# Kernel tuning notes

Measured on AMD Instinct MI355X. Metric: run time of the kernel, lower is better.

The kernel has to match this reference:

```python
import jax, jax.numpy as jnp
import numpy as np

B, C, H, Wd = 4, 144, 64, 64
CM = 64          # mid channels (planes[1..3])
K, PAD = 5, 2    # proj_kernel_size unfold
EPS = 1e-5       # BatchNorm eps


def _bn(x, g, b, m, v, axis=1):
    sh = [1] * x.ndim
    sh[axis] = -1
    return (x - m.reshape(sh)) * (g.reshape(sh) * jax.lax.rsqrt(v.reshape(sh) + EPS)) + b.reshape(sh)


def setup_inputs():
    key = jax.random.key(0)
    ks = jax.random.split(key, 24)
    def w(k, shape, s=0.1):
        return jax.random.normal(k, shape, dtype=jnp.float32) * s
    inp = {
        'x': jax.random.normal(ks[0], (B, C, H, Wd), dtype=jnp.float32),
        'w_in': w(ks[1], (CM, C)),
        'g_in': 1.0 + w(ks[2], (CM,)), 'b_in': w(ks[3], (CM,)),
        'm_in': w(ks[4], (CM,)), 'v_in': jax.random.uniform(ks[5], (CM,), minval=0.5, maxval=1.5),
        'w1': w(ks[6], (CM, CM, 3, 3)),
        'g1': 1.0 + w(ks[7], (CM,)), 'b1': w(ks[8], (CM,)),
        'm1': w(ks[9], (CM,)), 'v1': jax.random.uniform(ks[10], (CM,), minval=0.5, maxval=1.5),
        'w2': w(ks[11], (CM, CM, 3, 3)),
        'g2': 1.0 + w(ks[12], (CM,)), 'b2': w(ks[13], (CM,)),
        'm2': w(ks[14], (CM,)), 'v2': jax.random.uniform(ks[15], (CM,), minval=0.5, maxval=1.5),
        'w_out': w(ks[16], (C, CM)),
        'g_out': 1.0 + w(ks[17], (C,)), 'b_out': w(ks[18], (C,)),
        'm_out': w(ks[19], (C,)), 'v_out': jax.random.uniform(ks[20], (C,), minval=0.5, maxval=1.5),
    }
    return inp


def _forward(x, w_in, g_in, b_in, m_in, v_in, w1, g1, b1, m1, v1,
             w2, g2, b2, m2, v2, w_out, g_out, b_out, m_out, v_out):
    b, c, h, wd = x.shape
    # F.normalize over channel dim (L2, eps=1e-12)
    x = x / jnp.maximum(jnp.sqrt(jnp.sum(x * x, axis=1, keepdims=True)), 1e-12)
    # 5x5 unfold (im2col), pad 2 -> patches [b, c, K*K, h, w] (row-major (kh,kw) like torch)
    xp = jnp.pad(x, ((0, 0), (0, 0), (PAD, PAD), (PAD, PAD)))
    patches = jnp.stack([xp[:, :, i:i + h, j:j + wd]
                         for i in range(K) for j in range(K)], axis=2)
    # elementwise correlation with center pixel, reorder -> [b, c, h*w, K*K]
    y = patches * x[:, :, None, :, :]
    y = jnp.moveaxis(y, 2, -1).reshape(b, c, h * wd, K * K)
    # conv1x1_in + BN + ReLU (1x1 conv == channel matmul)
    z = jnp.einsum('oc,bcpk->bopk', w_in, y)
    z = jax.nn.relu(_bn(z, g_in, b_in, m_in, v_in, axis=1))
    cm = z.shape[1]
    # Conv3d kernel (1,3,3) VALID == 2D 3x3 conv per spatial position: fold h*w into batch
    z = z.reshape(b, cm, h * wd, K, K).transpose(0, 2, 1, 3, 4).reshape(b * h * wd, cm, K, K)
    dn = ('NCHW', 'OIHW', 'NCHW')
    z = jax.lax.conv_general_dilated(z, w1, (1, 1), 'VALID', dimension_numbers=dn)
    z = jax.nn.relu(_bn(z, g1, b1, m1, v1, axis=1))  # [b*hw, cm, 3, 3]
    z = jax.lax.conv_general_dilated(z, w2, (1, 1), 'VALID', dimension_numbers=dn)
    z = jax.nn.relu(_bn(z, g2, b2, m2, v2, axis=1))  # [b*hw, cm, 1, 1]
    z = z.reshape(b, h * wd, cm).transpose(0, 2, 1).reshape(b, cm, h, wd)
    # conv1x1_out + BN (final layer: no ReLU)
    out = jnp.einsum('oc,bchw->bohw', w_out, z)
    return _bn(out, g_out, b_out, m_out, v_out, axis=1)


def reference(x, w_in, g_in, b_in, m_in, v_in, w1, g1, b1, m1, v1,
              w2, g2, b2, m2, v2, w_out, g_out, b_out, m_out, v_out):
    return _forward(x, w_in, g_in, b_in, m_in, v_in, w1, g1, b1, m1, v1,
                    w2, g2, b2, m2, v2, w_out, g_out, b_out, m_out, v_out)
```

## Files before the change

### kernel.cpp

```cpp
#include <hip/hip_runtime.h>

#define BB   4
#define CC   144
#define HW   4096
#define PTOT 16384
#define EPSB 1e-5f

typedef __bf16 bf16;
typedef __bf16 bf16x8 __attribute__((ext_vector_type(8)));
typedef float  f32x4  __attribute__((ext_vector_type(4)));
typedef unsigned short U16;
typedef U16 u16x4 __attribute__((ext_vector_type(4)));
typedef U16 u16x8 __attribute__((ext_vector_type(8)));

#define MFMA __builtin_amdgcn_mfma_f32_16x16x32_bf16

#define XN_OFF    0UL
#define WINF_OFF  76021760UL
#define W1F_OFF   76042240UL
#define W2F_OFF   76115968UL
#define WOUTF_OFF 76189696UL
#define BNP_OFF   76208128UL

__global__ __launch_bounds__(576) void k_prep(const float* __restrict__ x,
    const float* __restrict__ w_in, const float* __restrict__ w1,
    const float* __restrict__ w2,   const float* __restrict__ w_out,
    const float* g_in, const float* b_in, const float* m_in, const float* v_in,
    const float* g1,   const float* b1,   const float* m1,   const float* v1,
    const float* g2,   const float* b2,   const float* m2,   const float* v2,
    const float* g_out,const float* b_out,const float* m_out,const float* v_out,
    bf16* xn2, bf16* w_inf, bf16* w1f, bf16* w2f, bf16* w_outf, float* bnp)
{
    __shared__ float red[9][64];
    if (blockIdx.x < 256) {
        int bh = blockIdx.x;
        int t = threadIdx.x, w = t & 63, cq = t >> 6;
        const float* px = x + ((size_t)(bh >> 6) * CC) * HW + (bh & 63) * 64 + w;
        float vals[16];
        float s = 0.f;
        #pragma unroll
        for (int i = 0; i < 16; i++) {
            float v = px[(size_t)(cq * 16 + i) * HW];
            vals[i] = v; s += v * v;
        }
        red[cq][w] = s;
        __syncthreads();
        float tot = 0.f;
        #pragma unroll
        for (int q = 0; q < 9; q++) tot += red[q][w];
        float inv = 1.f / fmaxf(sqrtf(tot), 1e-12f);
        size_t p = (size_t)bh * 64 + w;
        #pragma unroll
        for (int k = 0; k < 2; k++) {
            int g = cq * 2 + k;
            u16x8 pk;
            #pragma unroll
            for (int j = 0; j < 8; j++) {
                bf16 v = (bf16)(vals[k * 8 + j] * inv);
                pk[j] = *(U16*)&v;
            }
            *(u16x8*)(xn2 + (((size_t)g) << 17) + p * 8) = pk;
        }
        return;
    }
    int t = (blockIdx.x - 256) * 576 + threadIdx.x;
    if (t < 10240) {
        int e = t, j = e & 7, lane = (e >> 3) & 63, r = e >> 9;
        int ks = r % 5, mt = r / 5;
        int o = mt * 16 + (lane & 15);
        int c = ks * 32 + ((lane >> 4) << 3) + j;
        float s = g_in[o] * rsqrtf(v_in[o] + EPSB);
        w_inf[e] = (c < 144) ? (bf16)(w_in[o * 144 + c] * s) : (bf16)0.f;
    } else if (t < 47104) {
        int e = t - 10240, j = e & 7, lane = (e >> 3) & 63, r = e >> 9;
        int ks = r % 18, mt = r / 18;
        int o = mt * 16 + (lane & 15);
        int k = ks * 32 + ((lane >> 4) << 3) + j;
        int ij = k >> 6, c = k & 63;
        float s = g1[o] * rsqrtf(v1[o] + EPSB);
        w1f[e] = (bf16)(w1[(o * 64 + c) * 9 + ij] * s);
    } else if (t < 83968) {
        int e = t - 47104, j = e & 7, lane = (e >> 3) & 63, r = e >> 9;
        int ks = r % 18, mt = r / 18;
        int o = mt * 16 + (lane & 15);
        int k = ks * 32 + ((lane >> 4) << 3) + j;
        int rs = k >> 6, c2 = k & 63;
        float s = g2[o] * rsqrtf(v2[o] + EPSB);
        w2f[e] = (bf16)(w2[o * 576 + c2 * 9 + rs] * s);
    } else if (t < 93184) {
        int e = t - 83968, j = e & 7, lane = (e >> 3) & 63, r = e >> 9;
        int ks = r & 1, mt = r >> 1;
        int o = mt * 16 + (lane & 15);
        int c = ks * 32 + ((lane >> 4) << 3) + j;
        float s = g_out[o] * rsqrtf(v_out[o] + EPSB);
        w_outf[e] = (bf16)(w_out[o * 64 + c] * s);
    } else if (t < 93856) {
        int i = t - 93184;
        const float *g, *bb, *mm, *vv; int c; bool is_t;
        if (i < 128)      { g=g_in; bb=b_in; mm=m_in; vv=v_in; c=i&63;        is_t=i>=64;  }
        else if (i < 256) { g=g1;   bb=b1;   mm=m1;   vv=v1;   c=(i-128)&63;  is_t=i>=192; }
        else if (i < 384) { g=g2;   bb=b2;   mm=m2;   vv=v2;   c=(i-256)&63;  is_t=i>=320; }
        else              { int ii=i-384; g=g_out; bb=b_out; mm=m_out; vv=v_out;
                            c = ii % 144; is_t = ii >= 144; }
        float s = g[c] * rsqrtf(vv[c] + EPSB);
        bnp[i] = is_t ? (bb[c] - mm[c] * s) : s;
    }
}

__global__ __launch_bounds__(256) void k_fused(const bf16* __restrict__ xn2,
        const bf16* __restrict__ w_inf, const bf16* __restrict__ w1f,
        const bf16* __restrict__ w2f,   const bf16* __restrict__ w_outf,
        const float* __restrict__ bnp,  float* __restrict__ out)
{
    __shared__ __align__(16) U16 lds[25600];
    U16* a2_lds = lds;
    U16* v3     = lds + 9216;

    const int LUT5c[9] = {0, 1, 2, 5, 6, 7, 10, 11, 12};

    int t = threadIdx.x, wid = t >> 6, lane = t & 63;
    int quad = lane >> 4, pl = lane & 15;
    int raw = blockIdx.x;
    int bid = (raw & 7) * 128 + (raw >> 3);
    int p0 = bid * 16;
    int b = p0 >> 12, h = (p0 >> 6) & 63, hw0 = p0 & 4095;
    int wc = (p0 & 63) + pl;

    bf16x8 af[4][5];
    #pragma unroll
    for (int mt = 0; mt < 4; mt++)
        #pragma unroll
        for (int ks = 0; ks < 5; ks++)
            af[mt][ks] = *(const bf16x8*)(w_inf + ((mt * 5 + ks) * 64 + lane) * 8);
    bf16x8 cfr[5];
    #pragma unroll
    for (int ks = 0; ks < 5; ks++) {
        int g = ks * 4 + quad;
        bf16x8 z = {};
        cfr[ks] = (g < 18) ? *(const bf16x8*)(xn2 + ((size_t)g << 17) + (size_t)(p0 + pl) * 8) : z;
    }
    f32x4 tv[4];
    #pragma unroll
    for (int mt = 0; mt < 4; mt++)
        tv[mt] = *(const f32x4*)&bnp[64 + mt * 16 + quad * 4];

    for (int kp = wid; kp < 25; kp += 4) {
        int kpr = kp / 5, kpc = kp - kpr * 5;
        int dh = kpr - 2, dw = kpc - 2;
        bool ok = ((unsigned)(h + dh) < 64u) && ((unsigned)(wc + dw) < 64u);
        size_t pn = (size_t)(p0 + dh * 64 + dw + pl);
        bf16x8 nv[5];
        #pragma unroll
        for (int ks = 0; ks < 5; ks++) {
            int g = ks * 4 + quad;
            bf16x8 z = {};
            nv[ks] = (ok && g < 18) ? *(const bf16x8*)(xn2 + ((size_t)g << 17) + pn * 8) : z;
        }
        f32x4 acc[4] = {};
        #pragma unroll
        for (int ks = 0; ks < 5; ks++) {
            bf16x8 bfr;
            #pragma unroll
            for (int j = 0; j < 8; j++)
                bfr[j] = (bf16)((float)nv[ks][j] * (float)cfr[ks][j]);
            #pragma unroll
            for (int mt = 0; mt < 4; mt++)
                acc[mt] = MFMA(af[mt][ks], bfr, acc[mt], 0, 0, 0);
        }
        int swb = kp * 3 + pl;
        #pragma unroll
        for (int mt = 0; mt < 4; mt++) {
            u16x4 pk;
            #pragma unroll
            for (int r = 0; r < 4; r++) {
                bf16 v = (bf16)fmaxf(acc[mt][r] + tv[mt][r], 0.f);
                pk[r] = *(U16*)&v;
            }
            int g0 = mt * 2 + (quad >> 1);
            int dst = pl * 1600 + kp * 64 + (((g0 + swb) & 7) << 3) + (quad & 1) * 4;
            *(u16x4*)&lds[dst] = pk;
        }
    }
    __syncthreads();

    u16x4 pk2[9];
    {
        int mt = wid;
        bf16x8 aaC[18];
        #pragma unroll
        for (int ks = 0; ks < 18; ks++)
            aaC[ks] = *(const bf16x8*)(w1f + ((mt * 18 + ks) * 64 + lane) * 8);
        f32x4 t1v = *(const f32x4*)&bnp[192 + mt * 16 + quad * 4];
        #pragma unroll
        for (int ch = 0; ch < 3; ch++) {
            f32x4 acc[3] = {};
            #pragma unroll
            for (int ks = 0; ks < 18; ks++) {
                int gb = (ks & 1) * 4 + quad;
                int l5 = LUT5c[ks >> 1];
                #pragma unroll
                for (int i = 0; i < 3; i++) {
                    int kpidx = l5 + LUT5c[ch * 3 + i];
                    int off = pl * 1600 + kpidx * 64 + (((gb + kpidx * 3 + pl) & 7) << 3);
                    bf16x8 bfr = *(const bf16x8*)&lds[off];
                    acc[i] = MFMA(aaC[ks], bfr, acc[i], 0, 0, 0);
                }
            }
            #pragma unroll
            for (int i = 0; i < 3; i++) {
                #pragma unroll
                for (int r = 0; r < 4; r++) {
                    bf16 v = (bf16)fmaxf(acc[i][r] + t1v[r], 0.f);
                    pk2[ch * 3 + i][r] = *(U16*)&v;
                }
            }
        }
    }
    __syncthreads();

    bf16x8 aaD[18];
    #pragma unroll
    for (int ks = 0; ks < 18; ks++)
        aaD[ks] = *(const bf16x8*)(w2f + ((wid * 18 + ks) * 64 + lane) * 8);
    {
        int mt = wid;
        #pragma unroll
        for (int rs = 0; rs < 9; rs++) {
            int c = rs * 8 + mt * 2 + (quad >> 1);
            int dst = pl * 576 + ((c >> 3) << 6) + ((((c & 7) + pl) & 7) << 3) + (quad & 1) * 4;
            *(u16x4*)&a2_lds[dst] = pk2[rs];
        }
    }
    __syncthreads();

    {
        int mt = wid;
        f32x4 acc3 = {};
        #pragma unroll
        for (int ks = 0; ks < 18; ks++) {
            int cg = ks * 4 + quad;
            int off = pl * 576 + ((cg >> 3) << 6) + ((((cg & 7) + pl) & 7) << 3);
            bf16x8 bfr = *(const bf16x8*)&a2_lds[off];
            acc3 = MFMA(aaD[ks], bfr, acc3, 0, 0, 0);
        }
        #pragma unroll
        for (int r = 0; r < 4; r++) {
            int o = mt * 16 + quad * 4 + r;
            bf16 yb = (bf16)fmaxf(acc3[r] + bnp[320 + o], 0.f);
            v3[pl * 64 + ((((o >> 3) + pl) & 7) << 3) + (o & 7)] = *(U16*)&yb;
        }
    }
    bf16x8 afrE[3][2];
    #pragma unroll
    for (int q = 0; q < 3; q++) {
        int mt = wid + q * 4;
        if (mt < 9) {
            afrE[q][0] = *(const bf16x8*)(w_outf + ((mt * 2 + 0) * 64 + lane) * 8);
            afrE[q][1] = *(const bf16x8*)(w_outf + ((mt * 2 + 1) * 64 + lane) * 8);
        }
    }
    __syncthreads();

    bf16x8 bfr0 = *(const bf16x8*)&v3[pl * 64 + (((quad + pl) & 7) << 3)];
    bf16x8 bfr1 = *(const bf16x8*)&v3[pl * 64 + ((((4 + quad) + pl) & 7) << 3)];
    #pragma unroll
    for (int q = 0; q < 3; q++) {
        int mt = wid + q * 4;
        if (mt < 9) {
            f32x4 accB = {};
            accB = MFMA(afrE[q][0], bfr0, accB, 0, 0, 0);
            accB = MFMA(afrE[q][1], bfr1, accB, 0, 0, 0);
            #pragma unroll
            for (int r = 0; r < 4; r++) {
                int oc = mt * 16 + quad * 4 + r;
                out[((size_t)(b * 144 + oc)) * 4096 + hw0 + pl] = accB[r] + bnp[528 + oc];
            }
        }
    }
}

extern "C" void kernel_launch(void* const* d_in, const int* in_sizes, int n_in,
                              void* d_out, int out_size, void* d_ws, size_t ws_size,
                              hipStream_t stream)
{
    const float* x     = (const float*)d_in[0];
    const float* w_in  = (const float*)d_in[1];
    const float* g_in  = (const float*)d_in[2];
    const float* b_in  = (const float*)d_in[3];
    const float* m_in  = (const float*)d_in[4];
    const float* v_in  = (const float*)d_in[5];
    const float* w1    = (const float*)d_in[6];
    const float* g1    = (const float*)d_in[7];
    const float* b1    = (const float*)d_in[8];
    const float* m1    = (const float*)d_in[9];
    const float* v1    = (const float*)d_in[10];
    const float* w2    = (const float*)d_in[11];
    const float* g2    = (const float*)d_in[12];
    const float* b2    = (const float*)d_in[13];
    const float* m2    = (const float*)d_in[14];
    const float* v2    = (const float*)d_in[15];
    const float* w_out = (const float*)d_in[16];
    const float* g_out = (const float*)d_in[17];
    const float* b_out = (const float*)d_in[18];
    const float* m_out = (const float*)d_in[19];
    const float* v_out = (const float*)d_in[20];
    float* out = (float*)d_out;

    char* ws = (char*)d_ws;
    bf16*  xn2    = (bf16*)(ws + XN_OFF);
    bf16*  w_inf  = (bf16*)(ws + WINF_OFF);
    bf16*  w1f    = (bf16*)(ws + W1F_OFF);
    bf16*  w2f    = (bf16*)(ws + W2F_OFF);
    bf16*  w_outf = (bf16*)(ws + WOUTF_OFF);
    float* bnp    = (float*)(ws + BNP_OFF);

    hipLaunchKernelGGL(k_prep, dim3(419), dim3(576), 0, stream,
                       x, w_in, w1, w2, w_out,
                       g_in, b_in, m_in, v_in, g1, b1, m1, v1,
                       g2, b2, m2, v2, g_out, b_out, m_out, v_out,
                       xn2, w_inf, w1f, w2f, w_outf, bnp);
    hipLaunchKernelGGL(k_fused, dim3(1024), dim3(256), 0, stream,
                       xn2, w_inf, w1f, w2f, w_outf, bnp, out);
}
```

Baseline: 128.3 us.

## Repartition conv1 work across waves by output position instead of channel tile

The 3x3 conv1 stage now assigns each wave a subset of the 9 output positions across all 4 channel tiles, instead of one channel tile across all positions. Wave 0 takes three positions and the others take two each. Each LDS B-fragment load is now reused across four MFMAs. Weight fragments are streamed with a 3-deep rotating prefetch rather than held as 18 preloaded registers, which lowers register pressure. The cost is an uneven load, since wave 0 does 12 MFMA chains per k-step against 8 for the other waves, plus more global weight loads per wave.

Result: slower. 136.0 us (+6.0%).

```diff
diff --git a/kernel.cpp b/kernel.cpp
--- a/kernel.cpp
+++ b/kernel.cpp
@@ -183,35 +183,55 @@
     }
     __syncthreads();
 
-    u16x4 pk2[9];
+    u16x4 pk2[12];
+    const int nsub    = (wid == 0) ? 12 : 8;
+    const int nrs     = (wid == 0) ? 3 : 2;
+    const int rs_base = (wid == 0) ? 0 : 2 * wid + 1;
     {
-        int mt = wid;
-        bf16x8 aaC[18];
-        #pragma unroll
-        for (int ks = 0; ks < 18; ks++)
-            aaC[ks] = *(const bf16x8*)(w1f + ((mt * 18 + ks) * 64 + lane) * 8);
-        f32x4 t1v = *(const f32x4*)&bnp[192 + mt * 16 + quad * 4];
-        #pragma unroll
-        for (int ch = 0; ch < 3; ch++) {
-            f32x4 acc[3] = {};
-            #pragma unroll
-            for (int ks = 0; ks < 18; ks++) {
-                int gb = (ks & 1) * 4 + quad;
-                int l5 = LUT5c[ks >> 1];
+        f32x4 accC[12] = {};
+        bf16x8 aA[3][4];
+        #pragma unroll
+        for (int mt = 0; mt < 4; mt++) {
+            aA[0][mt] = *(const bf16x8*)(w1f + ((mt * 18 + 0) * 64 + lane) * 8);
+            aA[1][mt] = *(const bf16x8*)(w1f + ((mt * 18 + 1) * 64 + lane) * 8);
+        }
+        #pragma unroll
+        for (int ks = 0; ks < 18; ks++) {
+            if (ks + 2 < 18) {
                 #pragma unroll
-                for (int i = 0; i < 3; i++) {
-                    int kpidx = l5 + LUT5c[ch * 3 + i];
+                for (int mt = 0; mt < 4; mt++)
+                    aA[(ks + 2) % 3][mt] =
+                        *(const bf16x8*)(w1f + ((mt * 18 + ks + 2) * 64 + lane) * 8);
+            }
+            int gb = (ks & 1) * 4 + quad;
+            int l5 = LUT5c[ks >> 1];
+            bf16x8 bfr[3];
+            #pragma unroll
+            for (int d = 0; d < 3; d++) {
+                if (d < nrs) {
+                    int rs = rs_base + d;
+                    int l5rs = rs + 2 * (rs / 3);
+                    int kpidx = l5 + l5rs;
                     int off = pl * 1600 + kpidx * 64 + (((gb + kpidx * 3 + pl) & 7) << 3);
-                    bf16x8 bfr = *(const bf16x8*)&lds[off];
-                    acc[i] = MFMA(aaC[ks], bfr, acc[i], 0, 0, 0);
+                    bfr[d] = *(const bf16x8*)&lds[off];
                 }
             }
             #pragma unroll
-            for (int i = 0; i < 3; i++) {
+            for (int u = 0; u < 12; u++)
+                if (u < nsub)
+                    accC[u] = MFMA(aA[ks % 3][u & 3], bfr[u >> 2], accC[u], 0, 0, 0);
+        }
+        f32x4 t1vC[4];
+        #pragma unroll
+        for (int mt = 0; mt < 4; mt++)
+            t1vC[mt] = *(const f32x4*)&bnp[192 + mt * 16 + quad * 4];
+        #pragma unroll
+        for (int u = 0; u < 12; u++) {
+            if (u < nsub) {
                 #pragma unroll
                 for (int r = 0; r < 4; r++) {
-                    bf16 v = (bf16)fmaxf(acc[i][r] + t1v[r], 0.f);
-                    pk2[ch * 3 + i][r] = *(U16*)&v;
+                    bf16 v = (bf16)fmaxf(accC[u][r] + t1vC[u & 3][r], 0.f);
+                    pk2[u][r] = *(U16*)&v;
                 }
             }
         }
@@ -222,13 +242,13 @@
     #pragma unroll
     for (int ks = 0; ks < 18; ks++)
         aaD[ks] = *(const bf16x8*)(w2f + ((wid * 18 + ks) * 64 + lane) * 8);
-    {
-        int mt = wid;
-        #pragma unroll
-        for (int rs = 0; rs < 9; rs++) {
+    #pragma unroll
+    for (int u = 0; u < 12; u++) {
+        if (u < nsub) {
+            int rs = rs_base + (u >> 2), mt = u & 3;
             int c = rs * 8 + mt * 2 + (quad >> 1);
             int dst = pl * 576 + ((c >> 3) << 6) + ((((c & 7) + pl) & 7) << 3) + (quad & 1) * 4;
-            *(u16x4*)&a2_lds[dst] = pk2[rs];
+            *(u16x4*)&a2_lds[dst] = pk2[u];
         }
     }
     __syncthreads();
```
